# Optimization experiments

Hardware: AMD Instinct MI355X
Metric: run time of the kernel (lower is better)

The kernel has to match this reference:

```python
import jax, jax.numpy as jnp
import numpy as np

NEG_SLOPE = 0.01  # F.leaky_relu default
FGW = 0.1         # feature_guidance_weight


def gat_layer(x, src, dst, W, att_l, att_r, heads, out_ch, concat):
    N = x.shape[0]
    # reward-based guidance weights (L1-normalized over nodes, F.normalize p=1 dim=0)
    rw = 1.0 / (jnp.abs(x[:, -1:]) + 1e-6)                    # [N,1]
    rw = rw / jnp.maximum(jnp.sum(jnp.abs(rw), axis=0), 1e-12)
    h = (x @ W).reshape(N, heads, out_ch)                      # [N,H,C]
    # per-node attention halves, gathered per edge (avoids [E,H,C] for scores)
    al = jnp.sum(h * att_l, axis=-1)                           # [N,H] (x_i side)
    ar = jnp.sum(h * att_r, axis=-1)                           # [N,H] (x_j side)
    alpha = jax.nn.leaky_relu(al[dst] + ar[src], NEG_SLOPE)    # [E,H]
    alpha = alpha + FGW * jnp.log(rw[src])                     # guidance from source node
    # segment softmax over incoming edges of each target node (PyG softmax)
    m = jax.ops.segment_max(alpha, dst, num_segments=N)        # [N,H]
    e = jnp.exp(alpha - m[dst])
    s = jax.ops.segment_sum(e, dst, num_segments=N)
    alpha = e / (s[dst] + 1e-16)                               # [E,H]
    # weighted scatter-aggregate of source features
    msg = h[src] * alpha[:, :, None]                           # [E,H,C]
    out = jax.ops.segment_sum(msg, dst, num_segments=N)        # [N,H,C]
    if concat:
        return out.reshape(N, heads * out_ch)
    return out.mean(axis=1)


def setup_inputs() -> dict:
    key = jax.random.key(0)
    ks = jax.random.split(key, 10)
    N, E, D_IN, HID, HEADS, D_OUT = 50000, 800000, 128, 64, 4, 1

    def xavier(k, shape, fan_in, fan_out):
        a = jnp.sqrt(6.0 / (fan_in + fan_out))
        return jax.random.uniform(k, shape, jnp.float32, -a, a)

    x = jax.random.normal(ks[0], (N, D_IN), jnp.float32)
    edge_index = jax.random.randint(ks[1], (2, E), 0, N, jnp.int32)
    W1 = xavier(ks[2], (D_IN, HEADS * HID), D_IN, HEADS * HID)
    att_l1 = xavier(ks[3], (1, HEADS, HID), HID, HID)
    att_r1 = xavier(ks[4], (1, HEADS, HID), HID, HID)
    W2 = xavier(ks[5], (HEADS * HID, HID), HEADS * HID, HID)
    att_l2 = xavier(ks[6], (1, 1, HID), HID, HID)
    att_r2 = xavier(ks[7], (1, 1, HID), HID, HID)
    fc_w = xavier(ks[8], (HID, D_OUT), HID, D_OUT)
    fc_b = jnp.zeros((D_OUT,), jnp.float32)
    return {"x": x, "edge_index": edge_index, "W1": W1, "att_l1": att_l1,
            "att_r1": att_r1, "W2": W2, "att_l2": att_l2, "att_r2": att_r2,
            "fc_w": fc_w, "fc_b": fc_b}


def reference(x, edge_index, W1, att_l1, att_r1, W2, att_l2, att_r2, fc_w, fc_b):
    src, dst = edge_index[0], edge_index[1]
    HID, HEADS = 64, 4
    h = gat_layer(x, src, dst, W1, att_l1, att_r1, HEADS, HID, concat=True)
    h = jax.nn.elu(h)  # dropout omitted (eval mode)
    h = gat_layer(h, src, dst, W2, att_l2, att_r2, 1, HID, concat=False)
    h = jax.nn.elu(h)
    return h @ fc_w + fc_b
```

## Files before the change

### kernel.cpp

```cpp
#include <hip/hip_runtime.h>
#include <hip/hip_bf16.h>

typedef __hip_bfloat16 bf16;
typedef __attribute__((ext_vector_type(8))) short bf16x8;
typedef __attribute__((ext_vector_type(4))) float f32x4;

#define NEG_SLOPE 0.01f
#define FGW 0.1f

__device__ __forceinline__ float b2f(bf16 v) { return __bfloat162float(v); }

__device__ __forceinline__ float ldf(const void* p, size_t i, int isbf) {
    return isbf ? b2f(((const bf16*)p)[i]) : ((const float*)p)[i];
}

__device__ __forceinline__ float bu2f(unsigned short u) {
    return __uint_as_float(((unsigned)u) << 16);
}
__device__ __forceinline__ unsigned short f2bu(float f) {
    return __bfloat16_as_ushort(__float2bfloat16(f));
}

__device__ __forceinline__ float waveReduceSum(float v) {
#pragma unroll
    for (int o = 32; o > 0; o >>= 1) v += __shfl_down(v, o, 64);
    return v;
}

#define ATOMIC_ADD_F32(p, v) unsafeAtomicAdd((p), (v))

__global__ __launch_bounds__(256) void k_degdet(const int* __restrict__ ei, int* __restrict__ deg, int E,
                                                const unsigned short* __restrict__ xr,
                                                float* __restrict__ sscal, int* __restrict__ flag,
                                                const void* __restrict__ W1, const void* __restrict__ W2,
                                                unsigned short* __restrict__ Wp1h,
                                                unsigned short* __restrict__ Wp1l,
                                                unsigned short* __restrict__ Wp2) {
    __shared__ int sflag;
    const int t = threadIdx.x;
    const bool packer = (blockIdx.x < 128);
    if (packer) {
        if (t < 64) {
            int big = 0;
            for (int i = t; i < 256; i += 64) {
                int ex = (xr[i] >> 7) & 0xFF;
                if (ex >= 0xBF) big = 1;
            }
            unsigned long long mk = __ballot(big);
            if (t == 0) sflag = (mk == 0ull) ? 1 : 0;
        }
        __syncthreads();
        const int isbf = sflag;
        if (blockIdx.x == 0 && t == 0) {
            *flag = isbf;
            sscal[0] = 0.f; sscal[1] = 0.f;
        }
        int id = blockIdx.x * 256 + t;
        {
            int j = id & 7, l = (id >> 3) & 63, ko = (id >> 9) & 3, T = id >> 11;
            int k = ko * 32 + (l >> 4) * 8 + j, col = T * 16 + (l & 15);
            float wv = ldf(W1, (size_t)k * 256 + col, isbf);
            unsigned short hi = f2bu(wv);
            Wp1h[id] = hi;
            Wp1l[id] = f2bu(wv - bu2f(hi));
        }
        if (id < 16384) {
            int j = id & 7, l = (id >> 3) & 63, ko = (id >> 9) & 7, T = id >> 12;
            int k = ko * 32 + (l >> 4) * 8 + j, col = T * 16 + (l & 15);
            Wp2[id] = f2bu(ldf(W2, (size_t)k * 64 + col, isbf));
        }
    }
    int e = blockIdx.x * 256 + t;
    if (e < E) atomicAdd(&deg[ei[E + e]], 1);
}

__global__ __launch_bounds__(256) void k_scanA(const int* __restrict__ deg, int* __restrict__ tmp,
                                               int* __restrict__ bsum, int N) {
    __shared__ int part[256];
    const int t = threadIdx.x;
    int i = blockIdx.x * 256 + t;
    int v = (i < N) ? deg[i] : 0;
    part[t] = v;
    __syncthreads();
    for (int o = 1; o < 256; o <<= 1) {
        int add = (t >= o) ? part[t - o] : 0;
        __syncthreads();
        part[t] += add;
        __syncthreads();
    }
    if (i < N) tmp[i] = part[t];
    if (t == 255) bsum[blockIdx.x] = part[255];
}

__global__ __launch_bounds__(256) void k_scanB(int* __restrict__ bsum, int nb, int* __restrict__ rowptrN) {
    __shared__ int part[256];
    const int t = threadIdx.x;
    const int K = (nb + 255) / 256;
    int vs[8];
    int lsum = 0;
#pragma unroll
    for (int k = 0; k < 8; k++) {
        int idx = t * K + k;
        vs[k] = (k < K && idx < nb) ? bsum[idx] : 0;
        lsum += vs[k];
    }
    part[t] = lsum;
    __syncthreads();
    for (int o = 1; o < 256; o <<= 1) {
        int add = (t >= o) ? part[t - o] : 0;
        __syncthreads();
        part[t] += add;
        __syncthreads();
    }
    int excl = part[t] - lsum;
#pragma unroll
    for (int k = 0; k < 8; k++) {
        int idx = t * K + k;
        if (k < K && idx < nb) { bsum[idx] = excl; excl += vs[k]; }
    }
    if (t == 255) *rowptrN = part[255];
}

__global__ __launch_bounds__(256) void k_scanC(const int* __restrict__ deg, const int* __restrict__ tmp,
                                               const int* __restrict__ bsum, int* __restrict__ rowptr,
                                               int* __restrict__ cursor, int N) {
    int i = blockIdx.x * 256 + threadIdx.x;
    if (i >= N) return;
    rowptr[i] = bsum[blockIdx.x] + tmp[i] - deg[i];
    cursor[i] = 0;
}

__global__ __launch_bounds__(256) void k_scatter(const int* __restrict__ ei, const int* __restrict__ rowptr,
                                                 int* __restrict__ cursor, int* __restrict__ csr_src, int E) {
    int e = blockIdx.x * 256 + threadIdx.x;
    if (e >= E) return;
    int d = ei[E + e];
    int pos = atomicAdd(&cursor[d], 1);
    csr_src[rowptr[d] + pos] = ei[e];
}

__global__ __launch_bounds__(256) void k_gemm1f(const void* __restrict__ x,
                                                const unsigned short* __restrict__ Wp1h,
                                                const unsigned short* __restrict__ Wp1l,
                                                const void* __restrict__ attl,
                                                const void* __restrict__ attr,
                                                unsigned short* __restrict__ h1,
                                                float* __restrict__ pk1,
                                                float* __restrict__ al1,
                                                float* __restrict__ rwS,
                                                int N, const int* __restrict__ flag) {
    const int isbf = *flag;
    __shared__ unsigned short Ash[64 * 136];
    __shared__ unsigned short Asl[64 * 136];
    __shared__ float rpart[64];
    const int row0 = blockIdx.x * 64;
    const int t = threadIdx.x;
    const int w = t >> 6, lane = t & 63;
    const int m = lane & 15, quad = lane >> 4;

#pragma unroll
    for (int it = 0; it < 4; it++) {
        int idx = it * 256 + t;
        int r = idx >> 4, c = idx & 15;
        float v[8];
        if (row0 + r < N) {
            if (isbf) {
                const unsigned short* xu = (const unsigned short*)x;
                uint4 raw = *reinterpret_cast<const uint4*>(xu + (size_t)(row0 + r) * 128 + c * 8);
                const unsigned short* rs = (const unsigned short*)&raw;
#pragma unroll
                for (int k = 0; k < 8; k++) v[k] = bu2f(rs[k]);
            } else {
                const float* xf = (const float*)x;
                float4 a = *reinterpret_cast<const float4*>(xf + (size_t)(row0 + r) * 128 + c * 8);
                float4 b = *reinterpret_cast<const float4*>(xf + (size_t)(row0 + r) * 128 + c * 8 + 4);
                v[0] = a.x; v[1] = a.y; v[2] = a.z; v[3] = a.w;
                v[4] = b.x; v[5] = b.y; v[6] = b.z; v[7] = b.w;
            }
        } else {
#pragma unroll
            for (int k = 0; k < 8; k++) v[k] = 0.f;
        }
        unsigned short hi[8], lo[8];
#pragma unroll
        for (int k = 0; k < 8; k++) {
            hi[k] = f2bu(v[k]);
            lo[k] = f2bu(v[k] - bu2f(hi[k]));
        }
        *reinterpret_cast<uint4*>(&Ash[r * 136 + c * 8]) = *reinterpret_cast<const uint4*>(hi);
        *reinterpret_cast<uint4*>(&Asl[r * 136 + c * 8]) = *reinterpret_cast<const uint4*>(lo);
    }
    __syncthreads();

    bf16x8 Bh[4][4];
#pragma unroll
    for (int tt = 0; tt < 4; tt++)
#pragma unroll
        for (int ko = 0; ko < 4; ko++)
            Bh[tt][ko] = *reinterpret_cast<const bf16x8*>(
                &Wp1h[(size_t)(((w * 4 + tt) * 4 + ko) * 64 + lane) * 8]);
    float avl[4], avr[4];
#pragma unroll
    for (int tt = 0; tt < 4; tt++) {
        int col = (w * 4 + tt) * 16 + m;
        avl[tt] = ldf(attl, col, isbf);
        avr[tt] = ldf(attr, col, isbf);
    }
    for (int sub = 0; sub < 4; sub++) {
        const int rbase = sub * 16;
        bf16x8 Ah[4], Al[4];
#pragma unroll
        for (int ko = 0; ko < 4; ko++) {
            Ah[ko] = *reinterpret_cast<const bf16x8*>(&Ash[(rbase + m) * 136 + ko * 32 + quad * 8]);
            Al[ko] = *reinterpret_cast<const bf16x8*>(&Asl[(rbase + m) * 136 + ko * 32 + quad * 8]);
        }
        f32x4 Cf[4];
#pragma unroll
        for (int tt = 0; tt < 4; tt++) Cf[tt] = (f32x4){0.f, 0.f, 0.f, 0.f};
#pragma unroll
        for (int ko = 0; ko < 4; ko++)
#pragma unroll
            for (int tt = 0; tt < 4; tt++) {
                Cf[tt] = __builtin_amdgcn_mfma_f32_16x16x32_bf16(Ah[ko], Bh[tt][ko], Cf[tt], 0, 0, 0);
                Cf[tt] = __builtin_amdgcn_mfma_f32_16x16x32_bf16(Al[ko], Bh[tt][ko], Cf[tt], 0, 0, 0);
                bf16x8 Bl = *reinterpret_cast<const bf16x8*>(
                    &Wp1l[(size_t)(((w * 4 + tt) * 4 + ko) * 64 + lane) * 8]);
                Cf[tt] = __builtin_amdgcn_mfma_f32_16x16x32_bf16(Ah[ko], Bl, Cf[tt], 0, 0, 0);
            }
#pragma unroll
        for (int tt = 0; tt < 4; tt++) {
            int col = (w * 4 + tt) * 16 + m;
#pragma unroll
            for (int reg = 0; reg < 4; reg++) {
                int row = row0 + rbase + quad * 4 + reg;
                if (row < N) h1[(size_t)row * 256 + col] = f2bu(Cf[tt][reg]);
            }
        }
        if (w == 3 && m == 15) {
#pragma unroll
            for (int reg = 0; reg < 4; reg++) {
                int row = row0 + rbase + quad * 4 + reg;
                if (row < N) pk1[(size_t)row * 8 + 5] = Cf[3][reg];
            }
        }
        float sl[4], sr[4];
#pragma unroll
        for (int reg = 0; reg < 4; reg++) {
            float a = 0.f, b = 0.f;
#pragma unroll
            for (int tt = 0; tt < 4; tt++) {
                a = fmaf(avl[tt], Cf[tt][reg], a);
                b = fmaf(avr[tt], Cf[tt][reg], b);
            }
            sl[reg] = a; sr[reg] = b;
        }
#pragma unroll
        for (int off = 8; off >= 1; off >>= 1) {
#pragma unroll
            for (int reg = 0; reg < 4; reg++) {
                sl[reg] += __shfl_down(sl[reg], off, 64);
                sr[reg] += __shfl_down(sr[reg], off, 64);
            }
        }
        if (m == 0) {
#pragma unroll
            for (int reg = 0; reg < 4; reg++) {
                int row = row0 + rbase + quad * 4 + reg;
                if (row < N) {
                    al1[(size_t)row * 4 + w] = sl[reg];
                    pk1[(size_t)row * 8 + w] = sr[reg];
                }
            }
        }
    }
    if (t < 64) {
        int row = row0 + t;
        float rr = 0.f;
        if (row < N) {
            float a = fabsf(ldf(x, (size_t)row * 128 + 127, isbf));
            rr = 1.f / (a + 1e-6f);
            pk1[(size_t)row * 8 + 4] = logf(rr);
        }
        rpart[t] = rr;
    }
    __syncthreads();
    if (t == 0) {
        float s = 0.f;
#pragma unroll
        for (int i = 0; i < 64; i++) s += rpart[i];
        ATOMIC_ADD_F32(rwS, s);
    }
}

__global__ __launch_bounds__(256) void k_agg1(const int* __restrict__ rowptr,
                                              const int* __restrict__ csr_src,
                                              const float* __restrict__ al1,
                                              const float* __restrict__ pk1,
                                              const float* __restrict__ rwS,
                                              const unsigned short* __restrict__ h1,
                                              unsigned short* __restrict__ x2b,
                                              float* __restrict__ x2c, int N) {
    int d = blockIdx.x * 4 + (threadIdx.x >> 6);
    if (d >= N) return;
    int lane = threadIdx.x & 63;
    int h = lane >> 4;
    const float gl = FGW * logf(fmaxf(*rwS, 1e-12f));
    float al_h = al1[d * 4 + h];
    int beg = rowptr[d], end = rowptr[d + 1];

    float s0 = 0.f, s1 = 0.f;
    float4 a0 = {0.f, 0.f, 0.f, 0.f}, a1 = {0.f, 0.f, 0.f, 0.f};

    auto load1 = [&](int idx, float& ar, float2& lc, uint2& hb) {
        int s = csr_src[idx];
        ar = pk1[(size_t)s * 8 + h];
        lc = *reinterpret_cast<const float2*>(&pk1[(size_t)s * 8 + 4]);
        hb = *reinterpret_cast<const uint2*>(&h1[(size_t)s * 256 + lane * 4]);
    };
    auto step = [&](float car, float2 clc, uint2 chb, float& s, float4& acc) {
        float a = al_h + car;
        a = fmaxf(a, NEG_SLOPE * a);
        a = fmaf(FGW, clc.x, a - gl);
        float e = __expf(a);
        s += e;
        float v0 = __uint_as_float(chb.x << 16);
        float v1 = __uint_as_float(chb.x & 0xFFFF0000u);
        float v2 = __uint_as_float(chb.y << 16);
        float v3 = __uint_as_float(chb.y & 0xFFFF0000u);
        v3 = (lane == 63) ? clc.y : v3;
        acc.x = fmaf(e, v0, acc.x);
        acc.y = fmaf(e, v1, acc.y);
        acc.z = fmaf(e, v2, acc.z);
        acc.w = fmaf(e, v3, acc.w);
    };

    if (beg < end) {
        int i = beg;
        if ((end - beg) & 1) {
            float ar; float2 lc; uint2 hb;
            load1(i, ar, lc, hb);
            step(ar, lc, hb, s0, a0);
            i++;
        }
        if (i < end) {
            float ar0, ar1v; float2 lc0, lc1; uint2 hb0, hb1;
            load1(i, ar0, lc0, hb0);
            load1(i + 1, ar1v, lc1, hb1);
            for (; i < end; i += 2) {
                float car0 = ar0, car1 = ar1v; float2 cl0 = lc0, cl1 = lc1;
                uint2 chb0 = hb0, chb1 = hb1;
                if (i + 2 < end) {
                    load1(i + 2, ar0, lc0, hb0);
                    load1(i + 3, ar1v, lc1, hb1);
                }
                step(car0, cl0, chb0, s0, a0);
                step(car1, cl1, chb1, s1, a1);
            }
        }
        s0 += s1;
        a0.x += a1.x; a0.y += a1.y; a0.z += a1.z; a0.w += a1.w;
    }
    float inv = 1.f / (s0 + 1e-16f);
    float4 o;
    o.x = a0.x * inv; o.y = a0.y * inv; o.z = a0.z * inv; o.w = a0.w * inv;
    o.x = (o.x > 0.f) ? o.x : expm1f(o.x);
    o.y = (o.y > 0.f) ? o.y : expm1f(o.y);
    o.z = (o.z > 0.f) ? o.z : expm1f(o.z);
    o.w = (o.w > 0.f) ? o.w : expm1f(o.w);
    uint2 ob;
    ob.x = (unsigned)f2bu(o.x) | ((unsigned)f2bu(o.y) << 16);
    ob.y = (unsigned)f2bu(o.z) | ((unsigned)f2bu(o.w) << 16);
    *reinterpret_cast<uint2*>(&x2b[(size_t)d * 256 + lane * 4]) = ob;
    if (lane == 63) x2c[d] = o.w;
}

__global__ __launch_bounds__(256) void k_gemm2f(const unsigned short* __restrict__ x2b,
                                                const float* __restrict__ x2c,
                                                const unsigned short* __restrict__ Wp2,
                                                const void* __restrict__ attl,
                                                const void* __restrict__ attr,
                                                unsigned short* __restrict__ h2,
                                                float* __restrict__ pk2,
                                                float* __restrict__ al2,
                                                float* __restrict__ rwS2,
                                                int N, const int* __restrict__ flag) {
    const int isbf = *flag;
    __shared__ unsigned short As[64 * 264];
    __shared__ float pl[4 * 64], pr[4 * 64], rpart[64];
    const int row0 = blockIdx.x * 64;
    const int t = threadIdx.x;
    const int w = t >> 6, lane = t & 63;
    const int m = lane & 15, quad = lane >> 4;
#pragma unroll
    for (int it = 0; it < 8; it++) {
        int idx = it * 256 + t;
        int r = idx >> 5, c = idx & 31;
        uint4 v = {0u, 0u, 0u, 0u};
        if (row0 + r < N)
            v = *reinterpret_cast<const uint4*>(x2b + (size_t)(row0 + r) * 256 + c * 8);
        *reinterpret_cast<uint4*>(&As[r * 264 + c * 8]) = v;
    }
    __syncthreads();
    bf16x8 Bf[8];
#pragma unroll
    for (int ko = 0; ko < 8; ko++)
        Bf[ko] = *reinterpret_cast<const bf16x8*>(&Wp2[(size_t)((w * 8 + ko) * 64 + lane) * 8]);
    f32x4 Cf[4];
#pragma unroll
    for (int sub = 0; sub < 4; sub++) Cf[sub] = (f32x4){0.f, 0.f, 0.f, 0.f};
#pragma unroll
    for (int ko = 0; ko < 8; ko++)
#pragma unroll
        for (int sub = 0; sub < 4; sub++) {
            bf16x8 Af = *reinterpret_cast<const bf16x8*>(
                &As[(sub * 16 + m) * 264 + ko * 32 + quad * 8]);
            Cf[sub] = __builtin_amdgcn_mfma_f32_16x16x32_bf16(Af, Bf[ko], Cf[sub], 0, 0, 0);
        }
    int col = w * 16 + m;
    float avl = ldf(attl, col, isbf);
    float avr = ldf(attr, col, isbf);
#pragma unroll
    for (int sub = 0; sub < 4; sub++) {
#pragma unroll
        for (int reg = 0; reg < 4; reg++) {
            int row = row0 + sub * 16 + quad * 4 + reg;
            if (row < N) h2[(size_t)row * 64 + col] = f2bu(Cf[sub][reg]);
        }
        float sl[4], sr[4];
#pragma unroll
        for (int reg = 0; reg < 4; reg++) { sl[reg] = avl * Cf[sub][reg]; sr[reg] = avr * Cf[sub][reg]; }
#pragma unroll
        for (int off = 8; off >= 1; off >>= 1) {
#pragma unroll
            for (int reg = 0; reg < 4; reg++) {
                sl[reg] += __shfl_down(sl[reg], off, 64);
                sr[reg] += __shfl_down(sr[reg], off, 64);
            }
        }
        if (m == 0) {
#pragma unroll
            for (int reg = 0; reg < 4; reg++) {
                pl[sub * 64 + w * 16 + quad * 4 + reg] = sl[reg];
                pr[sub * 64 + w * 16 + quad * 4 + reg] = sr[reg];
            }
        }
    }
    __syncthreads();
    if (t < 64) {
        int row = row0 + t;
        int sub = t >> 4, ri = t & 15;
        float rr = 0.f;
        if (row < N) {
            al2[row] = pl[sub * 64 + ri] + pl[sub * 64 + 16 + ri] + pl[sub * 64 + 32 + ri] + pl[sub * 64 + 48 + ri];
            pk2[(size_t)row * 2] = pr[sub * 64 + ri] + pr[sub * 64 + 16 + ri] + pr[sub * 64 + 32 + ri] + pr[sub * 64 + 48 + ri];
            float a = fabsf(x2c[row]);
            rr = 1.f / (a + 1e-6f);
            pk2[(size_t)row * 2 + 1] = logf(rr);
        }
        rpart[t] = rr;
    }
    __syncthreads();
    if (t == 0) {
        float s = 0.f;
#pragma unroll
        for (int i = 0; i < 64; i++) s += rpart[i];
        ATOMIC_ADD_F32(rwS2, s);
    }
}

__global__ __launch_bounds__(256) void k_agg2(const int* __restrict__ rowptr,
                                              const int* __restrict__ csr_src,
                                              const float* __restrict__ al2,
                                              const float* __restrict__ pk2,
                                              const float* __restrict__ rwS2,
                                              const unsigned short* __restrict__ h2,
                                              const void* __restrict__ fcw,
                                              const void* __restrict__ fcb,
                                              void* __restrict__ y, int N,
                                              const int* __restrict__ flag) {
    const int isbf = *flag;
    int d = blockIdx.x * 4 + (threadIdx.x >> 6);
    if (d >= N) return;
    int lane = threadIdx.x & 63;
    const float gl2 = FGW * logf(fmaxf(*rwS2, 1e-12f));
    float al_d = al2[d];
    int beg = rowptr[d], end = rowptr[d + 1];

    float s0 = 0.f, acc0 = 0.f, s1 = 0.f, acc1 = 0.f;

    auto load1 = [&](int idx, float2& pv, float& hv) {
        int s = csr_src[idx];
        pv = *reinterpret_cast<const float2*>(&pk2[(size_t)s * 2]);
        hv = bu2f(h2[(size_t)s * 64 + lane]);
    };
    auto step = [&](float2 cpv, float ch, float& s, float& acc) {
        float a = al_d + cpv.x;
        a = fmaxf(a, NEG_SLOPE * a);
        a = fmaf(FGW, cpv.y, a - gl2);
        float e = __expf(a);
        s += e;
        acc = fmaf(e, ch, acc);
    };

    if (beg < end) {
        int i = beg;
        if ((end - beg) & 1) {
            float2 pv; float hv;
            load1(i, pv, hv);
            step(pv, hv, s0, acc0);
            i++;
        }
        if (i < end) {
            float2 pv0, pv1; float hv0, hv1;
            load1(i, pv0, hv0);
            load1(i + 1, pv1, hv1);
            for (; i < end; i += 2) {
                float2 cp0 = pv0, cp1 = pv1; float ch0 = hv0, ch1 = hv1;
                if (i + 2 < end) {
                    load1(i + 2, pv0, hv0);
                    load1(i + 3, pv1, hv1);
                }
                step(cp0, ch0, s0, acc0);
                step(cp1, ch1, s1, acc1);
            }
        }
        s0 += s1;
        acc0 += acc1;
    }
    float v = acc0 / (s0 + 1e-16f);
    v = (v > 0.f) ? v : expm1f(v);
    float r = waveReduceSum(v * ldf(fcw, lane, isbf));
    if (lane == 0) {
        float o = r + ldf(fcb, 0, isbf);
        if (isbf) ((bf16*)y)[d] = __float2bfloat16(o);
        else      ((float*)y)[d] = o;
    }
}

extern "C" void kernel_launch(void* const* d_in, const int* in_sizes, int n_in,
                              void* d_out, int out_size, void* d_ws, size_t ws_size,
                              hipStream_t stream) {
    const void* x     = d_in[0];
    const int*  ei    = (const int*)d_in[1];
    const void* W1    = d_in[2];
    const void* attl1 = d_in[3];
    const void* attr1 = d_in[4];
    const void* W2    = d_in[5];
    const void* attl2 = d_in[6];
    const void* attr2 = d_in[7];
    const void* fcw   = d_in[8];
    const void* fcb   = d_in[9];

    const int N = in_sizes[0] / 128;
    const int E = in_sizes[1] / 2;
    const int NB = (N + 255) / 256;

    float* p = (float*)d_ws;
    unsigned short* h1 = (unsigned short*)p; p += (size_t)N * 128;
    float* pk1    = p; p += (size_t)N * 8;
    float* al1    = p; p += (size_t)N * 4;
    unsigned short* x2b = (unsigned short*)p; p += (size_t)N * 128;
    float* x2c    = p; p += (size_t)N;
    float* pk2    = p; p += (size_t)N * 2;
    float* al2    = p; p += (size_t)N;
    int* rowptr   = (int*)p; p += (size_t)N + 1;
    int* deg      = (int*)p; p += (size_t)N;
    int* cursor   = (int*)p; p += (size_t)N;
    int* stmp     = (int*)p; p += (size_t)N;
    int* bsum     = (int*)p; p += (size_t)NB;
    int* csr_src  = (int*)p; p += (size_t)E;
    p = (float*)(((uintptr_t)p + 15) & ~(uintptr_t)15);
    unsigned short* Wp1h = (unsigned short*)p; p += 16384;
    unsigned short* Wp1l = (unsigned short*)p; p += 16384;
    unsigned short* Wp2  = (unsigned short*)p; p += 8192;
    float* sscal  = p; p += 4;
    int* dflag = (int*)(sscal + 2);

    unsigned short* h2 = h1;

    hipMemsetAsync(deg, 0, (size_t)N * 4, stream);

    k_degdet<<<(E + 255) / 256, 256, 0, stream>>>(ei, deg, E, (const unsigned short*)x, sscal, dflag,
                                                  W1, W2, Wp1h, Wp1l, Wp2);
    k_scanA<<<NB, 256, 0, stream>>>(deg, stmp, bsum, N);
    k_scanB<<<1, 256, 0, stream>>>(bsum, NB, &rowptr[N]);
    k_scanC<<<NB, 256, 0, stream>>>(deg, stmp, bsum, rowptr, cursor, N);
    k_scatter<<<(E + 255) / 256, 256, 0, stream>>>(ei, rowptr, cursor, csr_src, E);

    k_gemm1f<<<(N + 63) / 64, 256, 0, stream>>>(x, Wp1h, Wp1l, attl1, attr1, h1, pk1, al1,
                                                &sscal[0], N, dflag);
    k_agg1<<<(N + 3) / 4, 256, 0, stream>>>(rowptr, csr_src, al1, pk1,
                                            &sscal[0], h1, x2b, x2c, N);

    k_gemm2f<<<(N + 63) / 64, 256, 0, stream>>>(x2b, x2c, Wp2, attl2, attr2, h2, pk2, al2,
                                                &sscal[1], N, dflag);
    k_agg2<<<(N + 3) / 4, 256, 0, stream>>>(rowptr, csr_src, al2, pk2,
                                            &sscal[1], h2, fcw, fcb, d_out, N, dflag);
}
```

Before: 358.7 us.

## Process four edges per wave in parallel in both GAT aggregation kernels

Both aggregation kernels now split each wave into four 16-lane groups, with each group handling a different edge at the same time. Each lane loads wider 32-byte (agg1) or 8-byte (agg2) chunks of the source feature row. Source indices are loaded cooperatively in chunks of 64 and broadcast with shuffles, and the partial sums are combined across groups with xor-shuffles at the end. This raises memory-level parallelism and cuts the number of serial gather iterations per node, at the cost of more registers (16 accumulators) and some lanes idling when a node has few edges.

```diff
diff --git a/kernel.cpp b/kernel.cpp
--- a/kernel.cpp
+++ b/kernel.cpp
@@ -302,76 +302,92 @@
                                               float* __restrict__ x2c, int N) {
     int d = blockIdx.x * 4 + (threadIdx.x >> 6);
     if (d >= N) return;
-    int lane = threadIdx.x & 63;
-    int h = lane >> 4;
+    const int lane = threadIdx.x & 63;
+    const int q = lane & 15;
+    const int g = lane >> 4;
+    const int h = q >> 2;
+    const bool last15 = (q == 15);
     const float gl = FGW * logf(fmaxf(*rwS, 1e-12f));
-    float al_h = al1[d * 4 + h];
-    int beg = rowptr[d], end = rowptr[d + 1];
-
-    float s0 = 0.f, s1 = 0.f;
-    float4 a0 = {0.f, 0.f, 0.f, 0.f}, a1 = {0.f, 0.f, 0.f, 0.f};
-
-    auto load1 = [&](int idx, float& ar, float2& lc, uint2& hb) {
-        int s = csr_src[idx];
-        ar = pk1[(size_t)s * 8 + h];
-        lc = *reinterpret_cast<const float2*>(&pk1[(size_t)s * 8 + 4]);
-        hb = *reinterpret_cast<const uint2*>(&h1[(size_t)s * 256 + lane * 4]);
-    };
-    auto step = [&](float car, float2 clc, uint2 chb, float& s, float4& acc) {
-        float a = al_h + car;
-        a = fmaxf(a, NEG_SLOPE * a);
-        a = fmaf(FGW, clc.x, a - gl);
-        float e = __expf(a);
-        s += e;
-        float v0 = __uint_as_float(chb.x << 16);
-        float v1 = __uint_as_float(chb.x & 0xFFFF0000u);
-        float v2 = __uint_as_float(chb.y << 16);
-        float v3 = __uint_as_float(chb.y & 0xFFFF0000u);
-        v3 = (lane == 63) ? clc.y : v3;
-        acc.x = fmaf(e, v0, acc.x);
-        acc.y = fmaf(e, v1, acc.y);
-        acc.z = fmaf(e, v2, acc.z);
-        acc.w = fmaf(e, v3, acc.w);
-    };
-
-    if (beg < end) {
-        int i = beg;
-        if ((end - beg) & 1) {
-            float ar; float2 lc; uint2 hb;
-            load1(i, ar, lc, hb);
-            step(ar, lc, hb, s0, a0);
-            i++;
-        }
-        if (i < end) {
-            float ar0, ar1v; float2 lc0, lc1; uint2 hb0, hb1;
-            load1(i, ar0, lc0, hb0);
-            load1(i + 1, ar1v, lc1, hb1);
-            for (; i < end; i += 2) {
-                float car0 = ar0, car1 = ar1v; float2 cl0 = lc0, cl1 = lc1;
-                uint2 chb0 = hb0, chb1 = hb1;
-                if (i + 2 < end) {
-                    load1(i + 2, ar0, lc0, hb0);
-                    load1(i + 3, ar1v, lc1, hb1);
-                }
-                step(car0, cl0, chb0, s0, a0);
-                step(car1, cl1, chb1, s1, a1);
-            }
-        }
-        s0 += s1;
-        a0.x += a1.x; a0.y += a1.y; a0.z += a1.z; a0.w += a1.w;
-    }
-    float inv = 1.f / (s0 + 1e-16f);
-    float4 o;
-    o.x = a0.x * inv; o.y = a0.y * inv; o.z = a0.z * inv; o.w = a0.w * inv;
-    o.x = (o.x > 0.f) ? o.x : expm1f(o.x);
-    o.y = (o.y > 0.f) ? o.y : expm1f(o.y);
-    o.z = (o.z > 0.f) ? o.z : expm1f(o.z);
-    o.w = (o.w > 0.f) ? o.w : expm1f(o.w);
+    const float al_h = al1[(size_t)d * 4 + h];
+    const int beg = rowptr[d], end = rowptr[d + 1];
+
+    float acc[16];
+#pragma unroll
+    for (int k = 0; k < 16; k++) acc[k] = 0.f;
+    float ssum = 0.f;
+
+    for (int base = beg; base < end; base += 64) {
+        const int lim = min(end - base, 64);
+        const int sv = csr_src[base + min(lane, lim - 1)];
+
+        int s; float ar; float2 lc; uint4 b0, b1; bool val;
+        auto loadstep = [&](int j) {
+            int idx = j + g;
+            val = idx < lim;
+            int ii = min(idx, lim - 1);
+            s = __shfl(sv, ii, 64);
+            ar = pk1[(size_t)s * 8 + h];
+            lc = *reinterpret_cast<const float2*>(&pk1[(size_t)s * 8 + 4]);
+            const uint4* hp = reinterpret_cast<const uint4*>(h1 + (size_t)s * 256 + q * 16);
+            b0 = hp[0];
+            b1 = hp[1];
+        };
+        loadstep(0);
+        for (int j = 0; j < lim; j += 4) {
+            const float car = ar; const float2 clc = lc;
+            const uint4 cb0 = b0, cb1 = b1; const bool cval = val;
+            if (j + 4 < lim) loadstep(j + 4);
+
+            float a = al_h + car;
+            a = fmaxf(a, NEG_SLOPE * a);
+            a = fmaf(FGW, clc.x, a - gl);
+            float e = cval ? __expf(a) : 0.f;
+            ssum += e;
+
+            unsigned uu; float lo, hi;
+            uu = cb0.x; lo = __uint_as_float(uu << 16); hi = __uint_as_float(uu & 0xFFFF0000u);
+            acc[0] = fmaf(e, lo, acc[0]);  acc[1] = fmaf(e, hi, acc[1]);
+            uu = cb0.y; lo = __uint_as_float(uu << 16); hi = __uint_as_float(uu & 0xFFFF0000u);
+            acc[2] = fmaf(e, lo, acc[2]);  acc[3] = fmaf(e, hi, acc[3]);
+            uu = cb0.z; lo = __uint_as_float(uu << 16); hi = __uint_as_float(uu & 0xFFFF0000u);
+            acc[4] = fmaf(e, lo, acc[4]);  acc[5] = fmaf(e, hi, acc[5]);
+            uu = cb0.w; lo = __uint_as_float(uu << 16); hi = __uint_as_float(uu & 0xFFFF0000u);
+            acc[6] = fmaf(e, lo, acc[6]);  acc[7] = fmaf(e, hi, acc[7]);
+            uu = cb1.x; lo = __uint_as_float(uu << 16); hi = __uint_as_float(uu & 0xFFFF0000u);
+            acc[8] = fmaf(e, lo, acc[8]);  acc[9] = fmaf(e, hi, acc[9]);
+            uu = cb1.y; lo = __uint_as_float(uu << 16); hi = __uint_as_float(uu & 0xFFFF0000u);
+            acc[10] = fmaf(e, lo, acc[10]); acc[11] = fmaf(e, hi, acc[11]);
+            uu = cb1.z; lo = __uint_as_float(uu << 16); hi = __uint_as_float(uu & 0xFFFF0000u);
+            acc[12] = fmaf(e, lo, acc[12]); acc[13] = fmaf(e, hi, acc[13]);
+            uu = cb1.w; lo = __uint_as_float(uu << 16); hi = __uint_as_float(uu & 0xFFFF0000u);
+            hi = last15 ? clc.y : hi;
+            acc[14] = fmaf(e, lo, acc[14]); acc[15] = fmaf(e, hi, acc[15]);
+        }
+    }
+
+#pragma unroll
+    for (int k = 0; k < 16; k++) {
+        acc[k] += __shfl_xor(acc[k], 16, 64);
+        acc[k] += __shfl_xor(acc[k], 32, 64);
+    }
+    ssum += __shfl_xor(ssum, 16, 64);
+    ssum += __shfl_xor(ssum, 32, 64);
+
+    const float inv = 1.f / (ssum + 1e-16f);
+    float o0 = (g == 0 ? acc[0] : g == 1 ? acc[4]  : g == 2 ? acc[8]  : acc[12]);
+    float o1 = (g == 0 ? acc[1] : g == 1 ? acc[5]  : g == 2 ? acc[9]  : acc[13]);
+    float o2 = (g == 0 ? acc[2] : g == 1 ? acc[6]  : g == 2 ? acc[10] : acc[14]);
+    float o3 = (g == 0 ? acc[3] : g == 1 ? acc[7]  : g == 2 ? acc[11] : acc[15]);
+    o0 *= inv; o1 *= inv; o2 *= inv; o3 *= inv;
+    o0 = (o0 > 0.f) ? o0 : expm1f(o0);
+    o1 = (o1 > 0.f) ? o1 : expm1f(o1);
+    o2 = (o2 > 0.f) ? o2 : expm1f(o2);
+    o3 = (o3 > 0.f) ? o3 : expm1f(o3);
     uint2 ob;
-    ob.x = (unsigned)f2bu(o.x) | ((unsigned)f2bu(o.y) << 16);
-    ob.y = (unsigned)f2bu(o.z) | ((unsigned)f2bu(o.w) << 16);
-    *reinterpret_cast<uint2*>(&x2b[(size_t)d * 256 + lane * 4]) = ob;
-    if (lane == 63) x2c[d] = o.w;
+    ob.x = (unsigned)f2bu(o0) | ((unsigned)f2bu(o1) << 16);
+    ob.y = (unsigned)f2bu(o2) | ((unsigned)f2bu(o3) << 16);
+    *reinterpret_cast<uint2*>(&x2b[(size_t)d * 256 + q * 16 + g * 4]) = ob;
+    if (lane == 63) x2c[d] = o3;
 }
 
 __global__ __launch_bounds__(256) void k_gemm2f(const unsigned short* __restrict__ x2b,
@@ -481,55 +497,61 @@
     const int isbf = *flag;
     int d = blockIdx.x * 4 + (threadIdx.x >> 6);
     if (d >= N) return;
-    int lane = threadIdx.x & 63;
+    const int lane = threadIdx.x & 63;
+    const int q = lane & 15;
+    const int g = lane >> 4;
     const float gl2 = FGW * logf(fmaxf(*rwS2, 1e-12f));
-    float al_d = al2[d];
-    int beg = rowptr[d], end = rowptr[d + 1];
-
-    float s0 = 0.f, acc0 = 0.f, s1 = 0.f, acc1 = 0.f;
-
-    auto load1 = [&](int idx, float2& pv, float& hv) {
-        int s = csr_src[idx];
-        pv = *reinterpret_cast<const float2*>(&pk2[(size_t)s * 2]);
-        hv = bu2f(h2[(size_t)s * 64 + lane]);
-    };
-    auto step = [&](float2 cpv, float ch, float& s, float& acc) {
-        float a = al_d + cpv.x;
-        a = fmaxf(a, NEG_SLOPE * a);
-        a = fmaf(FGW, cpv.y, a - gl2);
-        float e = __expf(a);
-        s += e;
-        acc = fmaf(e, ch, acc);
-    };
-
-    if (beg < end) {
-        int i = beg;
-        if ((end - beg) & 1) {
-            float2 pv; float hv;
-            load1(i, pv, hv);
-            step(pv, hv, s0, acc0);
-            i++;
-        }
-        if (i < end) {
-            float2 pv0, pv1; float hv0, hv1;
-            load1(i, pv0, hv0);
-            load1(i + 1, pv1, hv1);
-            for (; i < end; i += 2) {
-                float2 cp0 = pv0, cp1 = pv1; float ch0 = hv0, ch1 = hv1;
-                if (i + 2 < end) {
-                    load1(i + 2, pv0, hv0);
-                    load1(i + 3, pv1, hv1);
-                }
-                step(cp0, ch0, s0, acc0);
-                step(cp1, ch1, s1, acc1);
-            }
-        }
-        s0 += s1;
-        acc0 += acc1;
-    }
-    float v = acc0 / (s0 + 1e-16f);
+    const float al_d = al2[d];
+    const int beg = rowptr[d], end = rowptr[d + 1];
+
+    float acc[4];
+#pragma unroll
+    for (int k = 0; k < 4; k++) acc[k] = 0.f;
+    float ssum = 0.f;
+
+    for (int base = beg; base < end; base += 64) {
+        const int lim = min(end - base, 64);
+        const int sv = csr_src[base + min(lane, lim - 1)];
+
+        int s; float2 pv; uint2 hb; bool val;
+        auto loadstep = [&](int j) {
+            int idx = j + g;
+            val = idx < lim;
+            int ii = min(idx, lim - 1);
+            s = __shfl(sv, ii, 64);
+            pv = *reinterpret_cast<const float2*>(&pk2[(size_t)s * 2]);
+            hb = *reinterpret_cast<const uint2*>(h2 + (size_t)s * 64 + q * 4);
+        };
+        loadstep(0);
+        for (int j = 0; j < lim; j += 4) {
+            const float2 cpv = pv; const uint2 chb = hb; const bool cval = val;
+            if (j + 4 < lim) loadstep(j + 4);
+
+            float a = al_d + cpv.x;
+            a = fmaxf(a, NEG_SLOPE * a);
+            a = fmaf(FGW, cpv.y, a - gl2);
+            float e = cval ? __expf(a) : 0.f;
+            ssum += e;
+            unsigned uu = chb.x;
+            acc[0] = fmaf(e, __uint_as_float(uu << 16), acc[0]);
+            acc[1] = fmaf(e, __uint_as_float(uu & 0xFFFF0000u), acc[1]);
+            uu = chb.y;
+            acc[2] = fmaf(e, __uint_as_float(uu << 16), acc[2]);
+            acc[3] = fmaf(e, __uint_as_float(uu & 0xFFFF0000u), acc[3]);
+        }
+    }
+
+#pragma unroll
+    for (int k = 0; k < 4; k++) {
+        acc[k] += __shfl_xor(acc[k], 16, 64);
+        acc[k] += __shfl_xor(acc[k], 32, 64);
+    }
+    ssum += __shfl_xor(ssum, 16, 64);
+    ssum += __shfl_xor(ssum, 32, 64);
+
+    float v = (g == 0 ? acc[0] : g == 1 ? acc[1] : g == 2 ? acc[2] : acc[3]) / (ssum + 1e-16f);
     v = (v > 0.f) ? v : expm1f(v);
-    float r = waveReduceSum(v * ldf(fcw, lane, isbf));
+    float r = waveReduceSum(v * ldf(fcw, q * 4 + g, isbf));
     if (lane == 0) {
         float o = r + ldf(fcb, 0, isbf);
         if (isbf) ((bf16*)y)[d] = __float2bfloat16(o);
```

Result: faster. 323.7 us (-9.7%).
